# Kernel tuning notes

Hardware: AMD Instinct MI355X
Metric: run time of the kernel (lower is better)

## Reference

```python
import jax, jax.numpy as jnp
import numpy as np

NUM_GAUSS = 64
MAX_R = 5.0
ANG_TO_NM = 0.1  # du.ANG_TO_NM_SCALE
L = 4
C_NODE = 256
C_HID = 256
MAX_ATOMS = 100
B = 512      # building blocks
NPB = 32     # atoms per block
K = 20       # max_neighbors
N = B * NPB
E = N * K
GAUSS_COEFF = -0.5 / (MAX_R / (NUM_GAUSS - 1)) ** 2


def setup_inputs() -> dict:
    rng = np.random.default_rng(0)
    # all atoms of a block inside a 2.5A cube -> every pair within MAX_R=5A,
    # so radius_graph capped at K neighbors == K-nearest graph (fixed E).
    pos = (rng.random((B, NPB, 3)) * 2.5).astype(np.float32)
    d = np.linalg.norm(pos[:, :, None, :] - pos[:, None, :, :], axis=-1)  # [B,n,n]
    ii = np.arange(NPB)
    d[:, ii, ii] = np.inf  # loop=False
    nbr = np.argsort(d, axis=-1)[:, :, :K]  # [B,n,K] nearest neighbors
    base = (np.arange(B) * NPB)[:, None, None]
    row = np.broadcast_to(ii[None, :, None], (B, NPB, K)) + base
    col = nbr + base
    edge_index = np.stack([row.reshape(-1), col.reshape(-1)]).astype(np.int64)

    key = jax.random.key(0)
    ks = jax.random.split(key, 8)

    def lin(k, fi, fo):
        return jax.random.normal(k, (L, fi, fo), jnp.float32) / np.sqrt(fi).astype(np.float32)

    d_e_in = 2 * C_NODE + 1 + NUM_GAUSS  # 577
    return {
        'local_coords': jnp.asarray(pos.reshape(N, 3)),
        'atom_types': jax.random.randint(ks[0], (N,), 1, MAX_ATOMS + 1),  # 1..max_atoms
        'edge_index': jnp.asarray(edge_index),
        'batch_bb': jnp.repeat(jnp.arange(B, dtype=jnp.int32), NPB),
        'atom_embed': jax.random.normal(ks[1], (MAX_ATOMS, C_NODE), jnp.float32) * 0.1,
        'offset': jnp.linspace(0.0, MAX_R, NUM_GAUSS, dtype=jnp.float32),
        'We1': lin(ks[2], d_e_in, C_HID), 'be1': jnp.zeros((L, C_HID), jnp.float32),
        'We2': lin(ks[3], C_HID, C_HID), 'be2': jnp.zeros((L, C_HID), jnp.float32),
        'Wn1': lin(ks[4], C_HID + C_NODE, C_HID), 'bn1': jnp.zeros((L, C_HID), jnp.float32),
        'Wn2': lin(ks[5], C_HID, C_NODE), 'bn2': jnp.zeros((L, C_NODE), jnp.float32),
    }


def _forward(local_coords, atom_types, edge_index, batch_bb, atom_embed, offset,
             We1, be1, We2, be2, Wn1, bn1, Wn2, bn2):
    row, col = edge_index[0], edge_index[1]
    h = atom_embed[atom_types - 1]                      # [N, C_NODE]
    # Gaussian smearing of pairwise distances (Angstrom)
    dvec = local_coords[col] - local_coords[row]        # [E, 3]
    dist = jnp.sqrt(jnp.sum(dvec * dvec, axis=-1))      # [E]
    edge_attr = jnp.exp(GAUSS_COEFF * (dist[:, None] - offset[None, :]) ** 2)  # [E, 64]
    coord = local_coords * ANG_TO_NM
    cdiff = coord[row] - coord[col]
    radial = jnp.sum(cdiff * cdiff, axis=-1, keepdims=True)  # [E, 1]
    nblocks = batch_bb.shape[0] // NPB  # static
    for l in range(L):  # small fixed layer count
        e_in = jnp.concatenate([h[row], h[col], radial, edge_attr], axis=-1)  # [E, 577]
        m = jax.nn.relu(e_in @ We1[l] + be1[l])
        m = jax.nn.relu(m @ We2[l] + be2[l])                 # edge_mlp output [E, C_HID]
        agg = jax.ops.segment_sum(m, row, num_segments=N)    # scatter-sum to nodes
        n_in = jnp.concatenate([h, agg], axis=-1)            # [N, C_NODE + C_HID]
        out = jax.nn.relu(n_in @ Wn1[l] + bn1[l]) @ Wn2[l] + bn2[l]
        node_update = h + out                                # residual inside E_GCL
        h = h + node_update                                  # outer residual in forward
    # global_mean_pool over building blocks
    s = jax.ops.segment_sum(h, batch_bb, num_segments=B)
    cnt = jax.ops.segment_sum(jnp.ones((h.shape[0], 1), h.dtype), batch_bb, num_segments=B)
    return s / cnt


def reference(local_coords, atom_types, edge_index, batch_bb, atom_embed, offset,
              We1, be1, We2, be2, Wn1, bn1, Wn2, bn2):
    return _forward(local_coords, atom_types, edge_index, batch_bb, atom_embed, offset,
                    We1, be1, We2, be2, Wn1, bn1, Wn2, bn2)
```

## Files before the change

kernel.cpp:

```cpp
#include <hip/hip_runtime.h>
#include <hip/hip_bf16.h>
#include <stdint.h>

#define NATOMS 16384
#define ETOT   327680
#define NLAYER 4

typedef __hip_bfloat16 bf16;
using bf16x8 = __attribute__((ext_vector_type(8))) short;
using f32x4  = __attribute__((ext_vector_type(4))) float;

#define LDSF_STRIDE 260
#define WBR_STRIDE  66

__device__ __forceinline__ float bf2f(short s) {
  union { float f; unsigned u; } x; x.u = ((unsigned)(unsigned short)s) << 16; return x.f;
}
__device__ __forceinline__ short f2bf(float f) {
  bf16 b = __float2bfloat16(f);
  return *(short*)&b;
}

__device__ __forceinline__ void async16(const void* g, void* l) {
  __builtin_amdgcn_global_load_lds(
      (const __attribute__((address_space(1))) unsigned int*)g,
      (__attribute__((address_space(3))) unsigned int*)l, 16, 0, 0);
}

template<int KTOT, int EPI, int MT>
__global__ void __launch_bounds__(256, 2)
gemm_k(const bf16* A, const bf16* A2, const bf16* B,
       bf16* Obf, int ldOut, const float* bias,
       float* Hf, bf16* Hbf)
{
  __shared__ __align__(16) char smem[49152];
  __shared__ float s_bias[256];

  const int tid  = threadIdx.x;
  const int w    = tid >> 6;
  const int lane = tid & 63;
  const int q    = lane >> 4;
  const int t16  = lane & 15;
  const size_t row0 = (size_t)blockIdx.x * MT;
  const int ncol0 = blockIdx.y * 256;
  constexpr int MI = MT / 16;
  constexpr int AI = MT / 32;

  if constexpr (EPI == 2 || EPI == 4) s_bias[tid] = bias[tid];

  f32x4 acc[MI][4] = {};

  constexpr int NCHUNK = KTOT / 64;
  for (int kc = 0; kc < NCHUNK; ++kc) {
    const int k0 = kc * 64;
    const bf16* Asrc; int k0e; int ldA;
    if constexpr (KTOT == 512) {
      if (k0 < 256) { Asrc = A;  k0e = k0;       }
      else          { Asrc = A2; k0e = k0 - 256; }
      ldA = 256;
    } else {
      Asrc = A; k0e = k0; ldA = KTOT;
    }

    __syncthreads();
    #pragma unroll
    for (int ii = 0; ii < AI; ++ii) {
      int i = w * AI + ii;
      int f = i * 64 + lane;
      int m = f >> 3, s = f & 7;
      int ko = s ^ (m & 7);
      const bf16* g = Asrc + (row0 + (size_t)m) * ldA + (size_t)(k0e + ko * 8);
      async16(g, smem + i * 1024);
    }
    #pragma unroll
    for (int ii = 0; ii < 8; ++ii) {
      int i = w * 8 + ii;
      int f = i * 64 + lane;
      int n = f >> 3, s = f & 7;
      int ko = s ^ (n & 7);
      const bf16* g = B + (size_t)(ncol0 + n) * KTOT + (size_t)(k0 + ko * 8);
      async16(g, smem + 16384 + i * 1024);
    }
    __syncthreads();

    #pragma unroll
    for (int ks = 0; ks < 2; ++ks) {
      bf16x8 av[MI]; bf16x8 bv[4];
      const int ko = q + 4 * ks;
      #pragma unroll
      for (int mi = 0; mi < MI; ++mi) {
        int m = 16 * mi + t16;
        int f = m * 8 + (ko ^ (m & 7));
        av[mi] = *(const bf16x8*)(smem + f * 16);
      }
      #pragma unroll
      for (int ni = 0; ni < 4; ++ni) {
        int n = 64 * w + 16 * ni + t16;
        int f = n * 8 + (ko ^ (n & 7));
        bv[ni] = *(const bf16x8*)(smem + 16384 + f * 16);
      }
      #pragma unroll
      for (int mi = 0; mi < MI; ++mi)
        #pragma unroll
        for (int ni = 0; ni < 4; ++ni)
          acc[mi][ni] = __builtin_amdgcn_mfma_f32_16x16x32_bf16(
              av[mi], bv[ni], acc[mi][ni], 0, 0, 0);
    }
  }

  float* lds_f = (float*)smem;
  #pragma unroll
  for (int mi = 0; mi < MI; ++mi) {
    __syncthreads();
    #pragma unroll
    for (int ni = 0; ni < 4; ++ni)
      #pragma unroll
      for (int r = 0; r < 4; ++r)
        lds_f[(4 * q + r) * LDSF_STRIDE + 64 * w + 16 * ni + t16] = acc[mi][ni][r];
    __syncthreads();
    #pragma unroll
    for (int j = 0; j < 2; ++j) {
      int task = tid + 256 * j;
      int rr = task >> 5, cg = task & 31;
      int c0 = cg * 8;
      size_t rg = row0 + 16 * mi + rr;
      f32x4 v0 = *(const f32x4*)(lds_f + rr * LDSF_STRIDE + c0);
      f32x4 v1 = *(const f32x4*)(lds_f + rr * LDSF_STRIDE + c0 + 4);
      float v[8] = {v0[0], v0[1], v0[2], v0[3], v1[0], v1[1], v1[2], v1[3]};
      if constexpr (EPI == 0) {
        bf16x8 o;
        #pragma unroll
        for (int k = 0; k < 8; ++k) o[k] = f2bf(v[k]);
        *(bf16x8*)(Obf + rg * ldOut + (ncol0 + c0)) = o;
      } else if constexpr (EPI == 2) {
        bf16x8 o;
        #pragma unroll
        for (int k = 0; k < 8; ++k) o[k] = f2bf(fmaxf(v[k] + s_bias[c0 + k], 0.f));
        *(bf16x8*)(Obf + rg * 256 + c0) = o;
      } else {
        f32x4 h0 = *(const f32x4*)(Hf + rg * 256 + c0);
        f32x4 h1 = *(const f32x4*)(Hf + rg * 256 + c0 + 4);
        float hh[8] = {h0[0], h0[1], h0[2], h0[3], h1[0], h1[1], h1[2], h1[3]};
        bf16x8 o; f32x4 n0, n1;
        #pragma unroll
        for (int k = 0; k < 8; ++k) {
          float hn = 2.f * hh[k] + v[k] + s_bias[c0 + k];
          o[k] = f2bf(hn);
          if (k < 4) n0[k] = hn; else n1[k - 4] = hn;
        }
        *(f32x4*)(Hf + rg * 256 + c0)     = n0;
        *(f32x4*)(Hf + rg * 256 + c0 + 4) = n1;
        *(bf16x8*)(Hbf + rg * 256 + c0) = o;
      }
    }
  }
}

__global__ void __launch_bounds__(256, 2)
gemm_edge1(const bf16* WgT_l, const float* off, const float* pos,
           const int* eidx, const bf16* Prc,
           const float* bias, const float* wrad, bf16* Om)
{
  __shared__ __align__(16) char smem[49152];
  __shared__ int   s_erow[128];
  __shared__ int   s_ecol[128];
  __shared__ float s_rad[128];
  __shared__ float s_dist[128];
  __shared__ float s_bias[256];
  __shared__ float s_wrad[256];
  __shared__ float s_off[64];

  const int tid  = threadIdx.x;
  const int w    = tid >> 6;
  const int lane = tid & 63;
  const int q    = lane >> 4;
  const int t16  = lane & 15;
  const int erow0 = blockIdx.x * 128;

  if (tid < 128) {
    int e = erow0 + tid;
    int r = eidx[e], c = eidx[ETOT + e];
    float dx = pos[c * 3 + 0] - pos[r * 3 + 0];
    float dy = pos[c * 3 + 1] - pos[r * 3 + 1];
    float dz = pos[c * 3 + 2] - pos[r * 3 + 2];
    float d2 = dx * dx + dy * dy + dz * dz;
    s_erow[tid] = r; s_ecol[tid] = c;
    s_rad[tid]  = 0.01f * d2;
    s_dist[tid] = sqrtf(d2);
  }
  if (tid < 64) s_off[tid] = off[tid];
  s_bias[tid] = bias[tid];
  s_wrad[tid] = wrad[tid];

  #pragma unroll
  for (int ii = 0; ii < 8; ++ii) {
    int i = w * 8 + ii;
    int f = i * 64 + lane;
    int n = f >> 3, s = f & 7;
    int ko = s ^ (n & 7);
    async16(WgT_l + (size_t)n * 64 + ko * 8, smem + 16384 + i * 1024);
  }
  __syncthreads();

  {
    const float GC = -0.5f / ((5.0f / 63.0f) * (5.0f / 63.0f));
    int m = tid >> 1, half = tid & 1;
    float d = s_dist[m];
    #pragma unroll
    for (int ko2 = 0; ko2 < 4; ++ko2) {
      int ko = half * 4 + ko2;
      bf16x8 v;
      #pragma unroll
      for (int j = 0; j < 8; ++j) {
        float t = d - s_off[ko * 8 + j];
        v[j] = f2bf(__expf(GC * t * t));
      }
      int f = m * 8 + (ko ^ (m & 7));
      *(bf16x8*)(smem + f * 16) = v;
    }
  }
  __syncthreads();

  f32x4 acc[8][4] = {};
  #pragma unroll
  for (int ks = 0; ks < 2; ++ks) {
    bf16x8 av[8]; bf16x8 bv[4];
    const int ko = q + 4 * ks;
    #pragma unroll
    for (int mi = 0; mi < 8; ++mi) {
      int m = 16 * mi + t16;
      int f = m * 8 + (ko ^ (m & 7));
      av[mi] = *(const bf16x8*)(smem + f * 16);
    }
    #pragma unroll
    for (int ni = 0; ni < 4; ++ni) {
      int n = 64 * w + 16 * ni + t16;
      int f = n * 8 + (ko ^ (n & 7));
      bv[ni] = *(const bf16x8*)(smem + 16384 + f * 16);
    }
    #pragma unroll
    for (int mi = 0; mi < 8; ++mi)
      #pragma unroll
      for (int ni = 0; ni < 4; ++ni)
        acc[mi][ni] = __builtin_amdgcn_mfma_f32_16x16x32_bf16(
            av[mi], bv[ni], acc[mi][ni], 0, 0, 0);
  }

  __syncthreads();
  float* br = (float*)(smem + 16384 + w * 4608);
  const int rs = lane >> 3, oct = lane & 7;
  const int c0e = 64 * w + oct * 8;
  float bias8[8], wrad8[8];
  #pragma unroll
  for (int k = 0; k < 8; ++k) { bias8[k] = s_bias[c0e + k]; wrad8[k] = s_wrad[c0e + k]; }

  #pragma unroll
  for (int mi = 0; mi < 8; ++mi) {
    #pragma unroll
    for (int ni = 0; ni < 4; ++ni)
      #pragma unroll
      for (int r = 0; r < 4; ++r)
        br[(4 * q + r) * WBR_STRIDE + 16 * ni + t16] = acc[mi][ni][r];
    #pragma unroll
    for (int pass = 0; pass < 2; ++pass) {
      int rr = pass * 8 + rs;
      int rl = 16 * mi + rr;
      int er = s_erow[rl], ec = s_ecol[rl];
      float rad = s_rad[rl];
      bf16x8 pr = *(const bf16x8*)(Prc + (size_t)er * 512 + c0e);
      bf16x8 pc = *(const bf16x8*)(Prc + (size_t)ec * 512 + 256 + c0e);
      float v[8];
      #pragma unroll
      for (int jj = 0; jj < 4; ++jj) {
        float2 t = *(const float2*)(br + rr * WBR_STRIDE + oct * 8 + 2 * jj);
        v[2 * jj] = t.x; v[2 * jj + 1] = t.y;
      }
      bf16x8 o;
      #pragma unroll
      for (int k = 0; k < 8; ++k) {
        float val = v[k] + bias8[k] + rad * wrad8[k] + bf2f(pr[k]) + bf2f(pc[k]);
        o[k] = f2bf(fmaxf(val, 0.f));
      }
      *(bf16x8*)(Om + ((size_t)(erow0 + rl)) * 256 + c0e) = o;
    }
  }
}

__global__ void __launch_bounds__(256, 2)
gemm_edge2agg(const bf16* M1, const bf16* We2T_l, const float* bias, bf16* Agg)
{
  __shared__ __align__(16) char smem[43008];
  __shared__ float s_bias[256];

  const int tid  = threadIdx.x;
  const int w    = tid >> 6;
  const int lane = tid & 63;
  const int q    = lane >> 4;
  const int t16  = lane & 15;
  const size_t erow0 = (size_t)blockIdx.x * 80;

  s_bias[tid] = bias[tid];

  f32x4 acc[5][4] = {};
  for (int kc = 0; kc < 4; ++kc) {
    const int k0 = kc * 64;
    __syncthreads();
    for (int i = w; i < 10; i += 4) {
      int f = i * 64 + lane;
      int m = f >> 3, s = f & 7;
      int ko = s ^ (m & 7);
      async16(M1 + (erow0 + (size_t)m) * 256 + (size_t)(k0 + ko * 8), smem + i * 1024);
    }
    #pragma unroll
    for (int ii = 0; ii < 8; ++ii) {
      int i = w * 8 + ii;
      int f = i * 64 + lane;
      int n = f >> 3, s = f & 7;
      int ko = s ^ (n & 7);
      async16(We2T_l + (size_t)n * 256 + (size_t)(k0 + ko * 8), smem + 10240 + i * 1024);
    }
    __syncthreads();

    #pragma unroll
    for (int ks = 0; ks < 2; ++ks) {
      bf16x8 av[5]; bf16x8 bv[4];
      const int ko = q + 4 * ks;
      #pragma unroll
      for (int mi = 0; mi < 5; ++mi) {
        int m = 16 * mi + t16;
        int f = m * 8 + (ko ^ (m & 7));
        av[mi] = *(const bf16x8*)(smem + f * 16);
      }
      #pragma unroll
      for (int ni = 0; ni < 4; ++ni) {
        int n = 64 * w + 16 * ni + t16;
        int f = n * 8 + (ko ^ (n & 7));
        bv[ni] = *(const bf16x8*)(smem + 10240 + f * 16);
      }
      #pragma unroll
      for (int mi = 0; mi < 5; ++mi)
        #pragma unroll
        for (int ni = 0; ni < 4; ++ni)
          acc[mi][ni] = __builtin_amdgcn_mfma_f32_16x16x32_bf16(
              av[mi], bv[ni], acc[mi][ni], 0, 0, 0);
    }
  }

  #pragma unroll
  for (int ni = 0; ni < 4; ++ni) {
    float b = s_bias[64 * w + 16 * ni + t16];
    float pp[5];
    #pragma unroll
    for (int mi = 0; mi < 5; ++mi) {
      float s = 0.f;
      #pragma unroll
      for (int r = 0; r < 4; ++r) s += fmaxf(acc[mi][ni][r] + b, 0.f);
      pp[mi] = s;
    }
    #pragma unroll
    for (int nn = 0; nn < 4; ++nn) {
      float s = 0.f;
      #pragma unroll
      for (int mi = 0; mi < 5; ++mi) {
        int g = 4 * mi + q;
        if (g >= 5 * nn && g <= 5 * nn + 4) s += pp[mi];
      }
      s += __shfl_xor(s, 16, 64);
      s += __shfl_xor(s, 32, 64);
      if (q == nn)
        Agg[((size_t)blockIdx.x * 4 + nn) * 256 + 64 * w + 16 * ni + t16] =
            __float2bfloat16(s);
    }
  }
}

__global__ void wrct_kernel(const float* We1, bf16* WrcT) {
  int idx = blockIdx.x * 256 + threadIdx.x;
  int k = idx & 255, np = (idx >> 8) & 511, l = idx >> 17;
  float v = (np < 256)
      ? We1[((size_t)l * 577 + k) * 256 + np]
      : We1[((size_t)l * 577 + 256 + k) * 256 + (np - 256)];
  WrcT[idx] = __float2bfloat16(v);
}
__global__ void wgt_kernel(const float* We1, bf16* WgT) {
  int idx = blockIdx.x * 256 + threadIdx.x;
  int k = idx & 63, n = (idx >> 6) & 255, l = idx >> 14;
  WgT[idx] = __float2bfloat16(We1[((size_t)l * 577 + 513 + k) * 256 + n]);
}
__global__ void wrad_kernel(const float* We1, float* wrad) {
  int idx = blockIdx.x * 256 + threadIdx.x;
  int n = idx & 255, l = idx >> 8;
  wrad[idx] = We1[((size_t)l * 577 + 512) * 256 + n];
}
__global__ void trans_kernel(const float* src, bf16* dst, int R, int C) {
  int idx = blockIdx.x * 256 + threadIdx.x;
  int k = idx % R, rest = idx / R;
  int n = rest % C, l = rest / C;
  dst[idx] = __float2bfloat16(src[((size_t)l * R + k) * C + n]);
}

__global__ void h0_kernel(const int* types, const float* emb, float* h, bf16* hbf) {
  int i = blockIdx.x, c = threadIdx.x;
  float v = emb[(size_t)(types[i] - 1) * 256 + c];
  h[(size_t)i * 256 + c] = v;
  hbf[(size_t)i * 256 + c] = __float2bfloat16(v);
}

__global__ void pool_kernel(const float* h, float* out) {
  int b = blockIdx.x, c = threadIdx.x;
  float s = 0.f;
  #pragma unroll
  for (int j = 0; j < 32; ++j) s += h[((size_t)b * 32 + j) * 256 + c];
  out[(size_t)b * 256 + c] = s * (1.0f / 32.0f);
}

extern "C" void kernel_launch(void* const* d_in, const int* in_sizes, int n_in,
                              void* d_out, int out_size, void* d_ws, size_t ws_size,
                              hipStream_t stream) {
  const float* pos   = (const float*)d_in[0];
  const int*   atype = (const int*)  d_in[1];
  const int*   eidx  = (const int*)  d_in[2];
  const float* emb   = (const float*)d_in[4];
  const float* off   = (const float*)d_in[5];
  const float* We1   = (const float*)d_in[6];
  const float* be1   = (const float*)d_in[7];
  const float* We2   = (const float*)d_in[8];
  const float* be2   = (const float*)d_in[9];
  const float* Wn1   = (const float*)d_in[10];
  const float* bn1   = (const float*)d_in[11];
  const float* Wn2   = (const float*)d_in[12];
  const float* bn2   = (const float*)d_in[13];
  float* out = (float*)d_out;

  size_t o = 0;
  auto carve = [&](size_t bytes) {
    void* p = (char*)d_ws + o;
    o += (bytes + 255) & ~(size_t)255;
    return p;
  };
  float* h     = (float*)carve((size_t)NATOMS * 256 * 4);
  bf16*  hbf   = (bf16*) carve((size_t)NATOMS * 256 * 2);
  bf16*  Prc   = (bf16*) carve((size_t)NATOMS * 512 * 2);
  bf16*  m1    = (bf16*) carve((size_t)ETOT * 256 * 2);
  bf16*  aggbf = (bf16*) carve((size_t)NATOMS * 256 * 2);
  bf16*  WrcT  = (bf16*) carve((size_t)NLAYER * 512 * 256 * 2);
  bf16*  WgT   = (bf16*) carve((size_t)NLAYER * 256 * 64 * 2);
  bf16*  We2T  = (bf16*) carve((size_t)NLAYER * 256 * 256 * 2);
  bf16*  Wn1T  = (bf16*) carve((size_t)NLAYER * 256 * 512 * 2);
  bf16*  Wn2T  = (bf16*) carve((size_t)NLAYER * 256 * 256 * 2);
  float* wradp = (float*)carve((size_t)NLAYER * 256 * 4);

  wrct_kernel<<<2048, 256, 0, stream>>>(We1, WrcT);
  wgt_kernel <<< 256, 256, 0, stream>>>(We1, WgT);
  wrad_kernel<<<   4, 256, 0, stream>>>(We1, wradp);
  trans_kernel<<<1024, 256, 0, stream>>>(We2, We2T, 256, 256);
  trans_kernel<<<2048, 256, 0, stream>>>(Wn1, Wn1T, 512, 256);
  trans_kernel<<<1024, 256, 0, stream>>>(Wn2, Wn2T, 256, 256);
  h0_kernel  <<<NATOMS, 256, 0, stream>>>(atype, emb, h, hbf);

  for (int l = 0; l < NLAYER; ++l) {
    gemm_k<256, 0, 64><<<dim3(256, 2), 256, 0, stream>>>(
        hbf, nullptr, WrcT + (size_t)l * 512 * 256, Prc, 512, nullptr,
        nullptr, nullptr);
    gemm_edge1<<<ETOT / 128, 256, 0, stream>>>(
        WgT + (size_t)l * 256 * 64, off, pos, eidx, Prc,
        be1 + l * 256, wradp + l * 256, m1);
    gemm_edge2agg<<<ETOT / 80, 256, 0, stream>>>(
        m1, We2T + (size_t)l * 256 * 256, be2 + l * 256, aggbf);
    gemm_k<512, 2, 64><<<dim3(256, 1), 256, 0, stream>>>(
        hbf, aggbf, Wn1T + (size_t)l * 256 * 512, aggbf, 256, bn1 + l * 256,
        nullptr, nullptr);
    gemm_k<256, 4, 64><<<dim3(256, 1), 256, 0, stream>>>(
        aggbf, nullptr, Wn2T + (size_t)l * 256 * 256, nullptr, 0, bn2 + l * 256,
        h, hbf);
  }

  pool_kernel<<<512, 256, 0, stream>>>(h, out);
}
```

Baseline: 710.4 us.

## Fuse the two edge-MLP GEMMs so the hidden layer stays in LDS

Merges gemm_edge1 and gemm_edge2agg into one edge_fused kernel that works on 80-edge tiles. The first layer's ReLU output is written to a swizzled LDS buffer and consumed directly by the second GEMM, so the ETOT x 256 bf16 intermediate (m1) is no longer written to and read back from global memory. The Gaussian A-fragments are now computed straight into registers rather than staged through LDS. In exchange the kernel uses about 72KB of static LDS, which may reduce occupancy below the requested two blocks per CU, and the smaller tile means the first-layer weights are loaded by more blocks.

```diff
diff --git a/kernel.cpp b/kernel.cpp
--- a/kernel.cpp
+++ b/kernel.cpp
@@ -156,18 +156,21 @@
   }
 }
 
+#define M1OFF 0
+#define BREG  40960
 __global__ void __launch_bounds__(256, 2)
-gemm_edge1(const bf16* WgT_l, const float* off, const float* pos,
-           const int* eidx, const bf16* Prc,
-           const float* bias, const float* wrad, bf16* Om)
+edge_fused(const bf16* WgT_l, const bf16* We2T_l, const float* off,
+           const float* pos, const int* eidx, const bf16* Prc,
+           const float* be1, const float* wrad, const float* be2, bf16* Agg)
 {
-  __shared__ __align__(16) char smem[49152];
-  __shared__ int   s_erow[128];
-  __shared__ int   s_ecol[128];
-  __shared__ float s_rad[128];
-  __shared__ float s_dist[128];
-  __shared__ float s_bias[256];
+  __shared__ __align__(16) char smem[73728];
+  __shared__ int   s_erow[80];
+  __shared__ int   s_ecol[80];
+  __shared__ float s_rad[80];
+  __shared__ float s_dist[80];
+  __shared__ float s_b1[256];
   __shared__ float s_wrad[256];
+  __shared__ float s_b2[256];
   __shared__ float s_off[64];
 
   const int tid  = threadIdx.x;
@@ -175,10 +178,10 @@
   const int lane = tid & 63;
   const int q    = lane >> 4;
   const int t16  = lane & 15;
-  const int erow0 = blockIdx.x * 128;
-
-  if (tid < 128) {
-    int e = erow0 + tid;
+  const size_t erow0 = (size_t)blockIdx.x * 80;
+
+  if (tid < 80) {
+    int e = (int)erow0 + tid;
     int r = eidx[e], c = eidx[ETOT + e];
     float dx = pos[c * 3 + 0] - pos[r * 3 + 0];
     float dy = pos[c * 3 + 1] - pos[r * 3 + 1];
@@ -189,8 +192,9 @@
     s_dist[tid] = sqrtf(d2);
   }
   if (tid < 64) s_off[tid] = off[tid];
-  s_bias[tid] = bias[tid];
+  s_b1[tid]   = be1[tid];
   s_wrad[tid] = wrad[tid];
+  s_b2[tid]   = be2[tid];
 
   #pragma unroll
   for (int ii = 0; ii < 8; ++ii) {
@@ -198,126 +202,102 @@
     int f = i * 64 + lane;
     int n = f >> 3, s = f & 7;
     int ko = s ^ (n & 7);
-    async16(WgT_l + (size_t)n * 64 + ko * 8, smem + 16384 + i * 1024);
+    async16(WgT_l + (size_t)n * 64 + ko * 8, smem + BREG + i * 1024);
   }
   __syncthreads();
 
-  {
-    const float GC = -0.5f / ((5.0f / 63.0f) * (5.0f / 63.0f));
-    int m = tid >> 1, half = tid & 1;
-    float d = s_dist[m];
-    #pragma unroll
-    for (int ko2 = 0; ko2 < 4; ++ko2) {
-      int ko = half * 4 + ko2;
-      bf16x8 v;
+  const float GC = -0.5f / ((5.0f / 63.0f) * (5.0f / 63.0f));
+  float offk[2][8];
+  #pragma unroll
+  for (int ks = 0; ks < 2; ++ks)
+    #pragma unroll
+    for (int j = 0; j < 8; ++j) offk[ks][j] = s_off[(q + 4 * ks) * 8 + j];
+
+  bf16x8 ag[5][2];
+  #pragma unroll
+  for (int mi = 0; mi < 5; ++mi) {
+    float d = s_dist[16 * mi + t16];
+    #pragma unroll
+    for (int ks = 0; ks < 2; ++ks)
       #pragma unroll
       for (int j = 0; j < 8; ++j) {
-        float t = d - s_off[ko * 8 + j];
-        v[j] = f2bf(__expf(GC * t * t));
-      }
-      int f = m * 8 + (ko ^ (m & 7));
-      *(bf16x8*)(smem + f * 16) = v;
-    }
-  }
-  __syncthreads();
-
-  f32x4 acc[8][4] = {};
+        float t = d - offk[ks][j];
+        ag[mi][ks][j] = f2bf(__expf(GC * t * t));
+      }
+  }
+
+  f32x4 acc1[5][4] = {};
   #pragma unroll
   for (int ks = 0; ks < 2; ++ks) {
-    bf16x8 av[8]; bf16x8 bv[4];
+    bf16x8 bv[4];
     const int ko = q + 4 * ks;
-    #pragma unroll
-    for (int mi = 0; mi < 8; ++mi) {
-      int m = 16 * mi + t16;
-      int f = m * 8 + (ko ^ (m & 7));
-      av[mi] = *(const bf16x8*)(smem + f * 16);
-    }
     #pragma unroll
     for (int ni = 0; ni < 4; ++ni) {
       int n = 64 * w + 16 * ni + t16;
       int f = n * 8 + (ko ^ (n & 7));
-      bv[ni] = *(const bf16x8*)(smem + 16384 + f * 16);
-    }
-    #pragma unroll
-    for (int mi = 0; mi < 8; ++mi)
+      bv[ni] = *(const bf16x8*)(smem + BREG + f * 16);
+    }
+    #pragma unroll
+    for (int mi = 0; mi < 5; ++mi)
       #pragma unroll
       for (int ni = 0; ni < 4; ++ni)
-        acc[mi][ni] = __builtin_amdgcn_mfma_f32_16x16x32_bf16(
-            av[mi], bv[ni], acc[mi][ni], 0, 0, 0);
-  }
-
+        acc1[mi][ni] = __builtin_amdgcn_mfma_f32_16x16x32_bf16(
+            ag[mi][ks], bv[ni], acc1[mi][ni], 0, 0, 0);
+  }
+
+  {
+    float* br = (float*)(smem + BREG + 8192 * w);
+    const int rs = lane >> 3, oct = lane & 7;
+    const int c0e = 64 * w + oct * 8;
+    float b18[8], wr8[8];
+    #pragma unroll
+    for (int k = 0; k < 8; ++k) { b18[k] = s_b1[c0e + k]; wr8[k] = s_wrad[c0e + k]; }
+
+    #pragma unroll
+    for (int mi = 0; mi < 5; ++mi) {
+      #pragma unroll
+      for (int ni = 0; ni < 4; ++ni)
+        #pragma unroll
+        for (int r = 0; r < 4; ++r)
+          br[(4 * q + r) * WBR_STRIDE + 16 * ni + t16] = acc1[mi][ni][r];
+      #pragma unroll
+      for (int pass = 0; pass < 2; ++pass) {
+        int rr = pass * 8 + rs;
+        int rl = 16 * mi + rr;
+        int er = s_erow[rl], ec = s_ecol[rl];
+        float rad = s_rad[rl];
+        bf16x8 pr = *(const bf16x8*)(Prc + (size_t)er * 512 + c0e);
+        bf16x8 pc = *(const bf16x8*)(Prc + (size_t)ec * 512 + 256 + c0e);
+        float v[8];
+        #pragma unroll
+        for (int jj = 0; jj < 4; ++jj) {
+          float2 t = *(const float2*)(br + rr * WBR_STRIDE + oct * 8 + 2 * jj);
+          v[2 * jj] = t.x; v[2 * jj + 1] = t.y;
+        }
+        bf16x8 o;
+        #pragma unroll
+        for (int k = 0; k < 8; ++k) {
+          float val = v[k] + b18[k] + rad * wr8[k] + bf2f(pr[k]) + bf2f(pc[k]);
+          o[k] = f2bf(fmaxf(val, 0.f));
+        }
+        int od = (8 * w + oct) ^ (rl & 7);
+        *(bf16x8*)(smem + rl * 512 + od * 16) = o;
+      }
+    }
+  }
   __syncthreads();
-  float* br = (float*)(smem + 16384 + w * 4608);
-  const int rs = lane >> 3, oct = lane & 7;
-  const int c0e = 64 * w + oct * 8;
-  float bias8[8], wrad8[8];
-  #pragma unroll
-  for (int k = 0; k < 8; ++k) { bias8[k] = s_bias[c0e + k]; wrad8[k] = s_wrad[c0e + k]; }
-
-  #pragma unroll
-  for (int mi = 0; mi < 8; ++mi) {
-    #pragma unroll
-    for (int ni = 0; ni < 4; ++ni)
-      #pragma unroll
-      for (int r = 0; r < 4; ++r)
-        br[(4 * q + r) * WBR_STRIDE + 16 * ni + t16] = acc[mi][ni][r];
-    #pragma unroll
-    for (int pass = 0; pass < 2; ++pass) {
-      int rr = pass * 8 + rs;
-      int rl = 16 * mi + rr;
-      int er = s_erow[rl], ec = s_ecol[rl];
-      float rad = s_rad[rl];
-      bf16x8 pr = *(const bf16x8*)(Prc + (size_t)er * 512 + c0e);
-      bf16x8 pc = *(const bf16x8*)(Prc + (size_t)ec * 512 + 256 + c0e);
-      float v[8];
-      #pragma unroll
-      for (int jj = 0; jj < 4; ++jj) {
-        float2 t = *(const float2*)(br + rr * WBR_STRIDE + oct * 8 + 2 * jj);
-        v[2 * jj] = t.x; v[2 * jj + 1] = t.y;
-      }
-      bf16x8 o;
-      #pragma unroll
-      for (int k = 0; k < 8; ++k) {
-        float val = v[k] + bias8[k] + rad * wrad8[k] + bf2f(pr[k]) + bf2f(pc[k]);
-        o[k] = f2bf(fmaxf(val, 0.f));
-      }
-      *(bf16x8*)(Om + ((size_t)(erow0 + rl)) * 256 + c0e) = o;
-    }
-  }
-}
-
-__global__ void __launch_bounds__(256, 2)
-gemm_edge2agg(const bf16* M1, const bf16* We2T_l, const float* bias, bf16* Agg)
-{
-  __shared__ __align__(16) char smem[43008];
-  __shared__ float s_bias[256];
-
-  const int tid  = threadIdx.x;
-  const int w    = tid >> 6;
-  const int lane = tid & 63;
-  const int q    = lane >> 4;
-  const int t16  = lane & 15;
-  const size_t erow0 = (size_t)blockIdx.x * 80;
-
-  s_bias[tid] = bias[tid];
-
-  f32x4 acc[5][4] = {};
+
+  f32x4 acc2[5][4] = {};
   for (int kc = 0; kc < 4; ++kc) {
-    const int k0 = kc * 64;
-    __syncthreads();
-    for (int i = w; i < 10; i += 4) {
-      int f = i * 64 + lane;
-      int m = f >> 3, s = f & 7;
-      int ko = s ^ (m & 7);
-      async16(M1 + (erow0 + (size_t)m) * 256 + (size_t)(k0 + ko * 8), smem + i * 1024);
-    }
+    if (kc) __syncthreads();
     #pragma unroll
     for (int ii = 0; ii < 8; ++ii) {
       int i = w * 8 + ii;
       int f = i * 64 + lane;
       int n = f >> 3, s = f & 7;
       int ko = s ^ (n & 7);
-      async16(We2T_l + (size_t)n * 256 + (size_t)(k0 + ko * 8), smem + 10240 + i * 1024);
+      async16(We2T_l + (size_t)n * 256 + (size_t)(64 * kc + ko * 8),
+              smem + BREG + i * 1024);
     }
     __syncthreads();
 
@@ -328,33 +308,33 @@
       #pragma unroll
       for (int mi = 0; mi < 5; ++mi) {
         int m = 16 * mi + t16;
-        int f = m * 8 + (ko ^ (m & 7));
-        av[mi] = *(const bf16x8*)(smem + f * 16);
+        int oa = (8 * kc + ko) ^ (t16 & 7);
+        av[mi] = *(const bf16x8*)(smem + m * 512 + oa * 16);
       }
       #pragma unroll
       for (int ni = 0; ni < 4; ++ni) {
         int n = 64 * w + 16 * ni + t16;
         int f = n * 8 + (ko ^ (n & 7));
-        bv[ni] = *(const bf16x8*)(smem + 10240 + f * 16);
+        bv[ni] = *(const bf16x8*)(smem + BREG + f * 16);
       }
       #pragma unroll
       for (int mi = 0; mi < 5; ++mi)
         #pragma unroll
         for (int ni = 0; ni < 4; ++ni)
-          acc[mi][ni] = __builtin_amdgcn_mfma_f32_16x16x32_bf16(
-              av[mi], bv[ni], acc[mi][ni], 0, 0, 0);
+          acc2[mi][ni] = __builtin_amdgcn_mfma_f32_16x16x32_bf16(
+              av[mi], bv[ni], acc2[mi][ni], 0, 0, 0);
     }
   }
 
   #pragma unroll
   for (int ni = 0; ni < 4; ++ni) {
-    float b = s_bias[64 * w + 16 * ni + t16];
+    float b = s_b2[64 * w + 16 * ni + t16];
     float pp[5];
     #pragma unroll
     for (int mi = 0; mi < 5; ++mi) {
       float s = 0.f;
       #pragma unroll
-      for (int r = 0; r < 4; ++r) s += fmaxf(acc[mi][ni][r] + b, 0.f);
+      for (int r = 0; r < 4; ++r) s += fmaxf(acc2[mi][ni][r] + b, 0.f);
       pp[mi] = s;
     }
     #pragma unroll
@@ -441,7 +421,6 @@
   float* h     = (float*)carve((size_t)NATOMS * 256 * 4);
   bf16*  hbf   = (bf16*) carve((size_t)NATOMS * 256 * 2);
   bf16*  Prc   = (bf16*) carve((size_t)NATOMS * 512 * 2);
-  bf16*  m1    = (bf16*) carve((size_t)ETOT * 256 * 2);
   bf16*  aggbf = (bf16*) carve((size_t)NATOMS * 256 * 2);
   bf16*  WrcT  = (bf16*) carve((size_t)NLAYER * 512 * 256 * 2);
   bf16*  WgT   = (bf16*) carve((size_t)NLAYER * 256 * 64 * 2);
@@ -462,11 +441,9 @@
     gemm_k<256, 0, 64><<<dim3(256, 2), 256, 0, stream>>>(
         hbf, nullptr, WrcT + (size_t)l * 512 * 256, Prc, 512, nullptr,
         nullptr, nullptr);
-    gemm_edge1<<<ETOT / 128, 256, 0, stream>>>(
-        WgT + (size_t)l * 256 * 64, off, pos, eidx, Prc,
-        be1 + l * 256, wradp + l * 256, m1);
-    gemm_edge2agg<<<ETOT / 80, 256, 0, stream>>>(
-        m1, We2T + (size_t)l * 256 * 256, be2 + l * 256, aggbf);
+    edge_fused<<<ETOT / 80, 256, 0, stream>>>(
+        WgT + (size_t)l * 256 * 64, We2T + (size_t)l * 256 * 256, off, pos,
+        eidx, Prc, be1 + l * 256, wradp + l * 256, be2 + l * 256, aggbf);
     gemm_k<512, 2, 64><<<dim3(256, 1), 256, 0, stream>>>(
         hbf, aggbf, Wn1T + (size_t)l * 256 * 512, aggbf, 256, bn1 + l * 256,
         nullptr, nullptr);
```

Result: faster. 645.4 us (-9.1%).
